# Optimization experiments

Hardware: AMD Instinct MI355X
Metric: run time of the kernel (lower is better)

## Reference

```python
import jax, jax.numpy as jnp
import numpy as np

C = 256   # channel
NH = 8    # n_heads
NP = 8    # n_points (n_levels = 1)
HD = C // NH


def conv1x1(x, W, b):
    # x: [B,C,H,W], W: [Cout,Cin] -> 1x1 conv == channel-mixing GEMM
    return jnp.einsum('bchw,oc->bohw', x, W) + b[None, :, None, None]


def linear(x, W, b):
    # x: [B,Q,Cin], W: [Cout,Cin] (torch nn.Linear layout)
    return jnp.einsum('bqc,oc->bqo', x, W) + b


def msda(value, loc, attn_w, H, Wd):
    # Multi-scale deformable attention core (single level).
    # value:  [B,Q,NH,HD]  (Q = H*Wd)
    # loc:    [B,Q,NH,NP,2] normalized sampling locations in [0,1] (x,y)
    # attn_w: [B,Q,NH,NP]  softmax weights
    B, Q = value.shape[0], value.shape[1]
    v = jnp.transpose(value, (0, 2, 1, 3))  # [B,NH,HW,HD]
    # grid_sample(align_corners=False): pixel coord = loc*size - 0.5
    ix = loc[..., 0] * Wd - 0.5
    iy = loc[..., 1] * H - 0.5
    x0 = jnp.floor(ix)
    y0 = jnp.floor(iy)

    def gather(xi, yi, wgt):
        valid = ((xi >= 0) & (xi < Wd) & (yi >= 0) & (yi < H)).astype(wgt.dtype)
        xc = jnp.clip(xi, 0, Wd - 1).astype(jnp.int32)
        yc = jnp.clip(yi, 0, H - 1).astype(jnp.int32)
        idx = yc * Wd + xc                                  # [B,Q,NH,NP]
        idx = jnp.transpose(idx, (0, 2, 1, 3)).reshape(B, NH, Q * NP)
        s = jnp.take_along_axis(v, idx[..., None], axis=2)  # [B,NH,Q*NP,HD]
        s = s.reshape(B, NH, Q, NP, HD)
        w = jnp.transpose(wgt * valid, (0, 2, 1, 3))[..., None]
        return s * w

    acc = (gather(x0, y0, (x0 + 1 - ix) * (y0 + 1 - iy))
           + gather(x0 + 1, y0, (ix - x0) * (y0 + 1 - iy))
           + gather(x0, y0 + 1, (x0 + 1 - ix) * (iy - y0))
           + gather(x0 + 1, y0 + 1, (ix - x0) * (iy - y0)))
    aw = jnp.transpose(attn_w, (0, 2, 1, 3))[..., None]      # [B,NH,Q,NP,1]
    out = (acc * aw).sum(axis=3)                             # [B,NH,Q,HD]
    return jnp.transpose(out, (0, 2, 1, 3)).reshape(B, Q, C)


def setup_inputs() -> dict:
    key = jax.random.key(0)
    ks = jax.random.split(key, 24)
    B, H, W = 2, 128, 128

    def w(k, shape, s=0.02):
        return jax.random.normal(k, shape, jnp.float32) * s

    d = {
        'xt': jax.random.normal(ks[0], (B, C, H, W), jnp.float32),
        'xt_1': jax.random.normal(ks[1], (B, C, H, W), jnp.float32),
        'W_in1': w(ks[2], (C, C)), 'b_in1': jnp.zeros((C,), jnp.float32),
        'W_in2': w(ks[3], (C, C)), 'b_in2': jnp.zeros((C,), jnp.float32),
        'Wv': w(ks[4], (C, C)), 'bv': jnp.zeros((C,), jnp.float32),
        'Ws': w(ks[5], (NH * NP * 2, C)), 'bs_off': w(ks[6], (NH * NP * 2,), 1.0),
        'Wa': w(ks[7], (NH * NP, C)), 'ba': jnp.zeros((NH * NP,), jnp.float32),
        'Wo': w(ks[8], (C, C)), 'bo': jnp.zeros((C,), jnp.float32),
        'Wt1': w(ks[9], (C, C)), 'bt1': jnp.zeros((C,), jnp.float32),
        'Wt2': w(ks[10], (C, C)), 'bt2': jnp.zeros((C,), jnp.float32),
        'Wout': w(ks[11], (C, C)), 'bout': jnp.zeros((C,), jnp.float32),
    }
    return d


def reference(xt, xt_1, W_in1, b_in1, W_in2, b_in2, Wv, bv, Ws, bs_off,
              Wa, ba, Wo, bo, Wt1, bt1, Wt2, bt2, Wout, bout):
    x1 = conv1x1(xt, W_in1, b_in1)
    x2 = conv1x1(xt_1, W_in2, b_in2)
    B, _, H, Wd = x1.shape
    Q = H * Wd
    q = jnp.transpose(x1, (0, 2, 3, 1)).reshape(B, Q, C)       # queries
    vflat = jnp.transpose(x2, (0, 2, 3, 1)).reshape(B, Q, C)   # values

    value = linear(vflat, Wv, bv).reshape(B, Q, NH, HD)
    offsets = linear(q, Ws, bs_off).reshape(B, Q, NH, NP, 2)
    attn = jax.nn.softmax(linear(q, Wa, ba).reshape(B, Q, NH, NP), axis=-1)

    # reference points at pixel centers, normalized (x,y)
    gy, gx = jnp.meshgrid(jnp.arange(H), jnp.arange(Wd), indexing='ij')
    ref = jnp.stack([(gx.reshape(-1) + 0.5) / Wd,
                     (gy.reshape(-1) + 0.5) / H], axis=-1).astype(jnp.float32)
    norm = jnp.array([Wd, H], jnp.float32)
    loc = ref[None, :, None, None, :] + offsets / norm          # [B,Q,NH,NP,2]

    out = msda(value, loc, attn, H, Wd)                         # [B,Q,C]
    xt_star = jnp.transpose(linear(out, Wo, bo), (0, 2, 1)).reshape(B, C, H, Wd)

    tg = conv1x1(jax.nn.relu(conv1x1(x1 * xt_star, Wt1, bt1)), Wt2, bt2)
    return jax.nn.relu(conv1x1(x1 + tg, Wout, bout))
```

## Files before the change

kernel.cpp:

```cpp
#include <hip/hip_runtime.h>
#include <math.h>


#define PIX 16384
#define BATCH 2
#define CH 256

typedef short bf16x8 __attribute__((ext_vector_type(8)));
typedef float f32x4 __attribute__((ext_vector_type(4)));

typedef const __attribute__((address_space(1))) void* as1cv;
typedef __attribute__((address_space(3))) void* as3v;
__device__ __forceinline__ void gl_lds16(const void* g, void* l) {
  __builtin_amdgcn_global_load_lds((as1cv)g, (as3v)l, 16, 0, 0);
}

__device__ __forceinline__ ushort f2bf(float f) {
  union { float f; unsigned u; } v; v.f = f;
  unsigned u = v.u;
  unsigned r = u + 0x7fffu + ((u >> 16) & 1u);
  return (ushort)(r >> 16);
}
__device__ __forceinline__ float bfl(unsigned u) {
  union { unsigned u; float f; } v; v.u = u << 16; return v.f;
}
__device__ __forceinline__ float bfh(unsigned u) {
  union { unsigned u; float f; } v; v.u = u & 0xffff0000u; return v.f;
}
__device__ __forceinline__ unsigned fuse_u32(unsigned a, unsigned b, bool mul) {
  float rl = mul ? bfl(a) * bfl(b) : bfl(a) + bfl(b);
  float rh = mul ? bfh(a) * bfh(b) : bfh(a) + bfh(b);
  return (unsigned)f2bf(rl) | ((unsigned)f2bf(rh) << 16);
}

__global__ __launch_bounds__(256) void wprep_k(
    const float* __restrict__ W_in1, const float* __restrict__ Wo,
    const float* __restrict__ Wt1, const float* __restrict__ Wt2,
    const float* __restrict__ Wout, const float* __restrict__ Ws,
    const float* __restrict__ Wa, const float* __restrict__ bs_off,
    const float* __restrict__ ba, ushort* __restrict__ wb,
    float* __restrict__ bsa)
{
  const int blk = blockIdx.x, k = threadIdx.x;
  if (blk >= 1472) {
    if (k < 128) bsa[k] = bs_off[k];
    else if (k < 192) bsa[k] = ba[k - 128];
    return;
  }
  const float* src;
  if (blk < 256) src = W_in1 + (size_t)blk * 256;
  else if (blk < 512) src = Wo + (size_t)(blk - 256) * 256;
  else if (blk < 768) src = Wt1 + (size_t)(blk - 512) * 256;
  else if (blk < 1024) src = Wt2 + (size_t)(blk - 768) * 256;
  else if (blk < 1280) src = Wout + (size_t)(blk - 1024) * 256;
  else if (blk < 1408) src = Ws + (size_t)(blk - 1280) * 256;
  else src = Wa + (size_t)(blk - 1408) * 256;
  wb[(size_t)blk * 256 + k] = f2bf(src[k]);
}

__global__ __launch_bounds__(256) void wvcomp_k(
    const float* __restrict__ Wv, const float* __restrict__ W_in2,
    const float* __restrict__ b_in2, const float* __restrict__ bv,
    ushort* __restrict__ Wvp, float* __restrict__ bvp)
{
  const int o = blockIdx.x, k = threadIdx.x;
  float acc = 0.f;
  #pragma unroll 8
  for (int c = 0; c < 256; ++c)
    acc += Wv[(size_t)o * 256 + c] * W_in2[(size_t)c * 256 + k];
  Wvp[(size_t)o * 256 + k] = f2bf(acc);
  __shared__ float red[256];
  red[k] = Wv[(size_t)o * 256 + k] * b_in2[k];
  __syncthreads();
  for (int s = 128; s > 0; s >>= 1) {
    if (k < s) red[k] += red[k + s];
    __syncthreads();
  }
  if (k == 0) bvp[o] = red[0] + bv[o];
}

__global__ __launch_bounds__(256) void tconv2_k(
    const float* __restrict__ inA, const float* __restrict__ inB,
    ushort* __restrict__ outA, ushort* __restrict__ outB)
{
  __shared__ float t[32][33];
  const int tid = threadIdx.x;
  const int z = blockIdx.z;
  const int b = z & 1;
  const float* in = (z < 2) ? inA : inB;
  ushort* out = (z < 2) ? outA : outB;
  const int p0 = blockIdx.x * 32, c0 = blockIdx.y * 32;
  const int tx = tid & 31, ty = tid >> 5;
  const float* inb = in + (size_t)b * CH * PIX;
  #pragma unroll
  for (int i = 0; i < 4; ++i)
    t[ty + i * 8][tx] = inb[(size_t)(c0 + ty + i * 8) * PIX + p0 + tx];
  __syncthreads();
  const int cx = (tid & 15) * 2, py = tid >> 4;
  ushort* outb = out + (size_t)b * PIX * CH;
  #pragma unroll
  for (int i = 0; i < 2; ++i) {
    int pl = py + i * 16;
    unsigned lo = f2bf(t[cx][pl]);
    unsigned hi = f2bf(t[cx + 1][pl]);
    *(unsigned*)(outb + (size_t)(p0 + pl) * CH + c0 + cx) = lo | (hi << 16);
  }
}

template<int FUSE, bool RELU, int OMODE>
__global__ __launch_bounds__(256, 3) void gemm2_k(
    const ushort* __restrict__ in, const ushort* __restrict__ in2,
    const ushort* __restrict__ Wb, const float* __restrict__ bias,
    void* __restrict__ out, int ldo, size_t obstride)
{
  __shared__ __align__(16) char smem[49152];
  const int tid = threadIdx.x;
  const int b = blockIdx.z;
  const int p0 = blockIdx.x * 128;
  const int o0 = blockIdx.y * 64;

  const ushort* inb = in + (size_t)b * PIX * CH;

  const int srow = tid >> 3, sseg = tid & 7;
  const int ssw = (srow & 7);
  const int gseg = (FUSE == 0) ? (sseg ^ ssw) : sseg;
  const ushort* xsrc = inb + (size_t)(p0 + srow) * CH + gseg * 8;
  const ushort* x2src = (FUSE != 0)
      ? in2 + (size_t)b * PIX * CH + (size_t)(p0 + srow) * CH + sseg * 8
      : (const ushort*)nullptr;
  const ushort* wsrc = Wb + (size_t)(o0 + srow) * CH + gseg * 8;

  const int l = tid & 63, wv = tid >> 6;
  const int lr = l & 15, g4 = l >> 4;

  f32x4 acc[2][4];
  #pragma unroll
  for (int i = 0; i < 2; ++i)
    #pragma unroll
    for (int j = 0; j < 4; ++j) acc[i][j] = (f32x4){0.f, 0.f, 0.f, 0.f};

  uint4 xr[4], x2r[4], wr[2];

#define STAGE_GLL(buf, kb)                                                     \
  {                                                                            \
    _Pragma("unroll")                                                          \
    for (int r = 0; r < 4; ++r)                                                \
      gl_lds16(xsrc + (kb) + (size_t)r * 32 * CH,                              \
               smem + (buf) * 16384 + r * 4096 + tid * 16);                    \
    _Pragma("unroll")                                                          \
    for (int r = 0; r < 2; ++r)                                                \
      gl_lds16(wsrc + (kb) + (size_t)r * 32 * CH,                              \
               smem + 32768 + (buf) * 8192 + r * 4096 + tid * 16);             \
  }

#define LOADT(kb)                                                              \
  {                                                                            \
    _Pragma("unroll")                                                          \
    for (int r = 0; r < 4; ++r)                                                \
      xr[r] = *(const uint4*)(xsrc + (kb) + (size_t)r * 32 * CH);              \
    _Pragma("unroll")                                                          \
    for (int r = 0; r < 4; ++r)                                                \
      x2r[r] = *(const uint4*)(x2src + (kb) + (size_t)r * 32 * CH);            \
    _Pragma("unroll")                                                          \
    for (int r = 0; r < 2; ++r)                                                \
      wr[r] = *(const uint4*)(wsrc + (kb) + (size_t)r * 32 * CH);              \
  }

#define WRITET(buf)                                                            \
  {                                                                            \
    _Pragma("unroll")                                                          \
    for (int r = 0; r < 4; ++r) {                                              \
      uint4 v = xr[r];                                                         \
      unsigned* pa = (unsigned*)&v;                                            \
      const unsigned* pb = (const unsigned*)&x2r[r];                           \
      _Pragma("unroll")                                                        \
      for (int w = 0; w < 4; ++w) pa[w] = fuse_u32(pa[w], pb[w], FUSE == 1);   \
      *(uint4*)(smem + (buf) * 16384 + (srow + r * 32) * 128 +                 \
                ((sseg ^ ssw) * 16)) = v;                                      \
    }                                                                          \
    _Pragma("unroll")                                                          \
    for (int r = 0; r < 2; ++r)                                                \
      *(uint4*)(smem + 32768 + (buf) * 8192 + (srow + r * 32) * 128 +          \
                ((sseg ^ ssw) * 16)) = wr[r];                                  \
  }

  if (FUSE == 0) { STAGE_GLL(0, 0) }
  else           { LOADT(0) WRITET(0) }
  __syncthreads();

  for (int t = 0; t < 4; ++t) {
    if (t < 3) {
      if (FUSE == 0) { STAGE_GLL((t + 1) & 1, (t + 1) * 64) }
      else           { LOADT((t + 1) * 64) }
    }
    const char* XB = smem + (t & 1) * 16384;
    const char* WB = smem + 32768 + (t & 1) * 8192;
    bf16x8 af[2][2], bfr[4][2];
    #pragma unroll
    for (int fm = 0; fm < 2; ++fm) {
      const int p = wv * 32 + fm * 16 + lr;
      #pragma unroll
      for (int kh = 0; kh < 2; ++kh)
        af[fm][kh] = *(const bf16x8*)(XB + p * 128 + (((kh * 4 + g4) ^ (p & 7)) * 16));
    }
    #pragma unroll
    for (int fn = 0; fn < 4; ++fn) {
      const int o = fn * 16 + lr;
      #pragma unroll
      for (int kh = 0; kh < 2; ++kh)
        bfr[fn][kh] = *(const bf16x8*)(WB + o * 128 + (((kh * 4 + g4) ^ (o & 7)) * 16));
    }
    #pragma unroll
    for (int fm = 0; fm < 2; ++fm)
      #pragma unroll
      for (int fn = 0; fn < 4; ++fn) {
        acc[fm][fn] = __builtin_amdgcn_mfma_f32_16x16x32_bf16(af[fm][0], bfr[fn][0], acc[fm][fn], 0, 0, 0);
        acc[fm][fn] = __builtin_amdgcn_mfma_f32_16x16x32_bf16(af[fm][1], bfr[fn][1], acc[fm][fn], 0, 0, 0);
      }
    if (t < 3 && FUSE != 0) { WRITET((t + 1) & 1) }
    __syncthreads();
  }
#undef STAGE_GLL
#undef LOADT
#undef WRITET

  float bvv[4];
  #pragma unroll
  for (int fn = 0; fn < 4; ++fn) bvv[fn] = bias[o0 + fn * 16 + lr];

  if (OMODE == 1) {
    float* El2 = (float*)smem;
    #pragma unroll
    for (int fm = 0; fm < 2; ++fm)
      #pragma unroll
      for (int fn = 0; fn < 4; ++fn) {
        float4 v;
        v.x = acc[fm][fn][0] + bvv[fn]; v.y = acc[fm][fn][1] + bvv[fn];
        v.z = acc[fm][fn][2] + bvv[fn]; v.w = acc[fm][fn][3] + bvv[fn];
        if (RELU) {
          v.x = fmaxf(v.x, 0.f); v.y = fmaxf(v.y, 0.f);
          v.z = fmaxf(v.z, 0.f); v.w = fmaxf(v.w, 0.f);
        }
        *(float4*)&El2[(size_t)(fn * 16 + lr) * 132 + wv * 32 + fm * 16 + g4 * 4] = v;
      }
    __syncthreads();
    float* outb = (float*)out + (size_t)b * obstride;
    const int og = tid >> 5, seg = tid & 31;
    #pragma unroll
    for (int r = 0; r < 8; ++r) {
      const int orow = og + r * 8;
      float4 v = *(float4*)(smem + orow * 528 + seg * 16);
      *(float4*)(outb + (size_t)(o0 + orow) * ldo + p0 + seg * 4) = v;
    }
  } else if (OMODE == 0) {
    ushort* El = (ushort*)smem;
    #pragma unroll
    for (int fm = 0; fm < 2; ++fm)
      #pragma unroll
      for (int fn = 0; fn < 4; ++fn)
        #pragma unroll
        for (int r = 0; r < 4; ++r) {
          const int p = wv * 32 + fm * 16 + g4 * 4 + r;
          float v = acc[fm][fn][r] + bvv[fn];
          if (RELU) v = fmaxf(v, 0.f);
          El[p * 72 + fn * 16 + lr] = f2bf(v);
        }
    __syncthreads();
    ushort* outb = (ushort*)out + (size_t)b * obstride;
    const int rg = tid >> 3, seg = tid & 7;
    #pragma unroll
    for (int r = 0; r < 4; ++r) {
      const int row = rg + r * 32;
      uint4 v = *(uint4*)(smem + row * 144 + seg * 16);
      *(uint4*)(outb + (size_t)(p0 + row) * ldo + o0 + seg * 8) = v;
    }
  } else {
    float* El = (float*)smem;
    #pragma unroll
    for (int fm = 0; fm < 2; ++fm)
      #pragma unroll
      for (int fn = 0; fn < 4; ++fn)
        #pragma unroll
        for (int r = 0; r < 4; ++r) {
          const int p = wv * 32 + fm * 16 + g4 * 4 + r;
          float v = acc[fm][fn][r] + bvv[fn];
          if (RELU) v = fmaxf(v, 0.f);
          El[p * 68 + fn * 16 + lr] = v;
        }
    __syncthreads();
    float* outb = (float*)out + (size_t)b * obstride;
    const int rg = tid >> 4, seg = tid & 15;
    #pragma unroll
    for (int r = 0; r < 8; ++r) {
      const int row = rg + r * 16;
      float4 v = *(float4*)(smem + row * 272 + seg * 16);
      *(float4*)(outb + (size_t)(p0 + row) * ldo + o0 + seg * 4) = v;
    }
  }
}

__global__ __launch_bounds__(256) void msda_k(
    const ushort* __restrict__ value, const float* __restrict__ sa,
    ushort* __restrict__ out)
{
  const int t = blockIdx.x * 256 + threadIdx.x;
  const int dh = t & 1;
  const int h = (t >> 1) & 7;
  const int pg = t >> 4;
  const int b = pg >> 14;
  const int p = pg & (PIX - 1);
  const int px = p & 127, py = p >> 7;

  const ushort* vb = value + (size_t)b * PIX * CH;
  const float* sp = sa + (size_t)pg * 192;

  float4 la = *(const float4*)(sp + 128 + h * 8);
  float4 lb = *(const float4*)(sp + 128 + h * 8 + 4);
  float lg[8] = {la.x, la.y, la.z, la.w, lb.x, lb.y, lb.z, lb.w};
  float m = lg[0];
  #pragma unroll
  for (int i = 1; i < 8; ++i) m = fmaxf(m, lg[i]);
  float s = 0.f;
  #pragma unroll
  for (int i = 0; i < 8; ++i) { lg[i] = __expf(lg[i] - m); s += lg[i]; }
  const float inv = 1.f / s;

  float of[16];
  #pragma unroll
  for (int j = 0; j < 4; ++j)
    *(float4*)&of[j * 4] = *(const float4*)(sp + h * 16 + j * 4);

  float acc[16];
  #pragma unroll
  for (int i = 0; i < 16; ++i) acc[i] = 0.f;

  #pragma unroll
  for (int pt = 0; pt < 8; ++pt) {
    const float ox = of[2 * pt], oy = of[2 * pt + 1];
    const float aw = lg[pt] * inv;
    const float ix = px + ox, iy = py + oy;
    const float xf = floorf(ix), yf = floorf(iy);
    const float fx = ix - xf, fy = iy - yf;
    const int x0 = (int)xf, y0 = (int)yf;
    #pragma unroll
    for (int cr = 0; cr < 4; ++cr) {
      const int dx = cr & 1, dy = cr >> 1;
      const int xx = x0 + dx, yy = y0 + dy;
      const float wx = dx ? fx : (1.f - fx);
      const float wy = dy ? fy : (1.f - fy);
      const bool valid = ((unsigned)xx < 128u) & ((unsigned)yy < 128u);
      float w = valid ? (wx * wy * aw) : 0.f;
      const int xc = min(max(xx, 0), 127), yc = min(max(yy, 0), 127);
      const ushort* vr = vb + ((size_t)(yc * 128 + xc) * CH + h * 32 + dh * 16);
      uint4 q0 = *(const uint4*)vr;
      uint4 q1 = *(const uint4*)(vr + 8);
      const unsigned* qw0 = (const unsigned*)&q0;
      const unsigned* qw1 = (const unsigned*)&q1;
      #pragma unroll
      for (int ww = 0; ww < 4; ++ww) {
        acc[2 * ww + 0] = fmaf(w, bfl(qw0[ww]), acc[2 * ww + 0]);
        acc[2 * ww + 1] = fmaf(w, bfh(qw0[ww]), acc[2 * ww + 1]);
        acc[8 + 2 * ww + 0] = fmaf(w, bfl(qw1[ww]), acc[8 + 2 * ww + 0]);
        acc[8 + 2 * ww + 1] = fmaf(w, bfh(qw1[ww]), acc[8 + 2 * ww + 1]);
      }
    }
  }
  unsigned r[8];
  #pragma unroll
  for (int k = 0; k < 8; ++k)
    r[k] = (unsigned)f2bf(acc[2 * k]) | ((unsigned)f2bf(acc[2 * k + 1]) << 16);
  ushort* dst = out + (size_t)pg * CH + h * 32 + dh * 16;
  *(uint4*)dst = *(uint4*)&r[0];
  *(uint4*)(dst + 8) = *(uint4*)&r[4];
}

extern "C" void kernel_launch(void* const* d_in, const int* in_sizes, int n_in,
                              void* d_out, int out_size, void* d_ws, size_t ws_size,
                              hipStream_t stream)
{
  const float* xt     = (const float*)d_in[0];
  const float* xt_1   = (const float*)d_in[1];
  const float* W_in1  = (const float*)d_in[2];
  const float* b_in1  = (const float*)d_in[3];
  const float* W_in2  = (const float*)d_in[4];
  const float* b_in2  = (const float*)d_in[5];
  const float* Wv     = (const float*)d_in[6];
  const float* bv     = (const float*)d_in[7];
  const float* Ws     = (const float*)d_in[8];
  const float* bs_off = (const float*)d_in[9];
  const float* Wa     = (const float*)d_in[10];
  const float* ba     = (const float*)d_in[11];
  const float* Wo     = (const float*)d_in[12];
  const float* bo     = (const float*)d_in[13];
  const float* Wt1    = (const float*)d_in[14];
  const float* bt1    = (const float*)d_in[15];
  const float* Wt2    = (const float*)d_in[16];
  const float* bt2    = (const float*)d_in[17];
  const float* Wout   = (const float*)d_in[18];
  const float* bout   = (const float*)d_in[19];

  char* ws = (char*)d_ws;
  const size_t SLOT = (size_t)BATCH * PIX * CH * 2;
  const size_t SAB  = (size_t)BATCH * PIX * 192 * 4;
  ushort* s0 = (ushort*)(ws + 0 * SLOT);
  ushort* s1 = (ushort*)(ws + 1 * SLOT);
  ushort* s2 = (ushort*)(ws + 2 * SLOT);
  ushort* s3 = (ushort*)(ws + 3 * SLOT);
  ushort* s4 = (ushort*)(ws + 4 * SLOT);
  float*  sa = (float*)(ws + 5 * SLOT);
  char* wbase = ws + 5 * SLOT + SAB;
  ushort* wb  = (ushort*)wbase;
  ushort* wvp = (ushort*)(wbase + (size_t)1472 * 256 * 2);
  float* bsa  = (float*)(wbase + (size_t)1472 * 256 * 2 + (size_t)256 * 256 * 2);
  float* bvp  = bsa + 192;

  ushort* wb_in1 = wb;
  ushort* wb_o   = wb + 65536;
  ushort* wb_t1  = wb + 131072;
  ushort* wb_t2  = wb + 196608;
  ushort* wb_out = wb + 262144;
  ushort* wb_sa  = wb + 327680;

  dim3 blk(256);
  dim3 gT(PIX / 32, CH / 32, 2 * BATCH);
  dim3 gF(PIX / 128, 4, BATCH);
  dim3 gS(PIX / 128, 3, BATCH);
  const size_t OBS = (size_t)PIX * CH;

  wprep_k<<<1473, blk, 0, stream>>>(W_in1, Wo, Wt1, Wt2, Wout, Ws, Wa, bs_off, ba, wb, bsa);
  wvcomp_k<<<256, blk, 0, stream>>>(Wv, W_in2, b_in2, bv, wvp, bvp);
  tconv2_k<<<gT, blk, 0, stream>>>(xt, xt_1, s0, s1);

  gemm2_k<0, false, 0><<<gF, blk, 0, stream>>>(s0, nullptr, wb_in1, b_in1, s2, CH, OBS);
  gemm2_k<0, false, 0><<<gF, blk, 0, stream>>>(s1, nullptr, wvp, bvp, s3, CH, OBS);
  gemm2_k<0, false, 2><<<gS, blk, 0, stream>>>(s2, nullptr, wb_sa, bsa, sa, 192, (size_t)PIX * 192);
  msda_k<<<dim3((BATCH * PIX * 16) / 256), blk, 0, stream>>>(s3, sa, s4);
  gemm2_k<0, false, 0><<<gF, blk, 0, stream>>>(s4, nullptr, wb_o, bo, s0, CH, OBS);
  gemm2_k<1, true , 0><<<gF, blk, 0, stream>>>(s0, s2, wb_t1, bt1, s1, CH, OBS);
  gemm2_k<0, false, 0><<<gF, blk, 0, stream>>>(s1, nullptr, wb_t2, bt2, s3, CH, OBS);
  gemm2_k<2, true , 1><<<gF, blk, 0, stream>>>(s3, s2, wb_out, bout, d_out, PIX, (size_t)CH * PIX);
}
```

Baseline: 164.9 us.

## Halve GEMM K-tile to cut LDS and store sampling params as bf16

The GEMM kernel moves from 64-wide to 32-wide K stages over eight iterations. This shrinks the shared-memory footprint with a matching swizzle, so four blocks per CU can be resident instead of three. Separately, the offset/attention-logit projection now writes bf16 instead of fp32, and msda_k decodes bf16 for those values. This halves that intermediate's traffic but lowers the precision of the sampling offsets and logits, and the shorter K stages add more barriers per block.

New measurement: 164.5 us. Within noise of the previous version (-0.2%).

```diff
diff --git a/kernel.cpp b/kernel.cpp
--- a/kernel.cpp
+++ b/kernel.cpp
@@ -108,12 +108,13 @@
 }
 
 template<int FUSE, bool RELU, int OMODE>
-__global__ __launch_bounds__(256, 3) void gemm2_k(
+__global__ __launch_bounds__(256, 4) void gemm2_k(
     const ushort* __restrict__ in, const ushort* __restrict__ in2,
     const ushort* __restrict__ Wb, const float* __restrict__ bias,
     void* __restrict__ out, int ldo, size_t obstride)
 {
-  __shared__ __align__(16) char smem[49152];
+  constexpr int SMEMSZ = (OMODE == 0) ? 24576 : 34816;
+  __shared__ __align__(16) char smem[SMEMSZ];
   const int tid = threadIdx.x;
   const int b = blockIdx.z;
   const int p0 = blockIdx.x * 128;
@@ -121,14 +122,19 @@
 
   const ushort* inb = in + (size_t)b * PIX * CH;
 
-  const int srow = tid >> 3, sseg = tid & 7;
-  const int ssw = (srow & 7);
-  const int gseg = (FUSE == 0) ? (sseg ^ ssw) : sseg;
-  const ushort* xsrc = inb + (size_t)(p0 + srow) * CH + gseg * 8;
-  const ushort* x2src = (FUSE != 0)
-      ? in2 + (size_t)b * PIX * CH + (size_t)(p0 + srow) * CH + sseg * 8
-      : (const ushort*)nullptr;
-  const ushort* wsrc = Wb + (size_t)(o0 + srow) * CH + gseg * 8;
+  const int srow = tid >> 2;
+  const int sseg = tid & 3;
+  const int swz0 = (srow >> 1) & 3;
+  const int swz1 = ((srow + 64) >> 1) & 3;
+  const int gseg0 = (FUSE == 0) ? (sseg ^ swz0) : sseg;
+  const int gseg1 = (FUSE == 0) ? (sseg ^ swz1) : sseg;
+  const ushort* xsrc0 = inb + (size_t)(p0 + srow) * CH + gseg0 * 8;
+  const ushort* xsrc1 = inb + (size_t)(p0 + srow + 64) * CH + gseg1 * 8;
+  const ushort* x2src0 = (FUSE != 0)
+      ? in2 + (size_t)b * PIX * CH + (size_t)(p0 + srow) * CH + sseg * 8 : (const ushort*)nullptr;
+  const ushort* x2src1 = (FUSE != 0)
+      ? in2 + (size_t)b * PIX * CH + (size_t)(p0 + srow + 64) * CH + sseg * 8 : (const ushort*)nullptr;
+  const ushort* wsrc = Wb + (size_t)(o0 + srow) * CH + gseg0 * 8;
 
   const int l = tid & 63, wv = tid >> 6;
   const int lr = l & 15, g4 = l >> 4;
@@ -139,85 +145,69 @@
     #pragma unroll
     for (int j = 0; j < 4; ++j) acc[i][j] = (f32x4){0.f, 0.f, 0.f, 0.f};
 
-  uint4 xr[4], x2r[4], wr[2];
+  uint4 xr[2], x2r[2], wr;
 
 #define STAGE_GLL(buf, kb)                                                     \
   {                                                                            \
-    _Pragma("unroll")                                                          \
-    for (int r = 0; r < 4; ++r)                                                \
-      gl_lds16(xsrc + (kb) + (size_t)r * 32 * CH,                              \
-               smem + (buf) * 16384 + r * 4096 + tid * 16);                    \
-    _Pragma("unroll")                                                          \
-    for (int r = 0; r < 2; ++r)                                                \
-      gl_lds16(wsrc + (kb) + (size_t)r * 32 * CH,                              \
-               smem + 32768 + (buf) * 8192 + r * 4096 + tid * 16);             \
+    gl_lds16(xsrc0 + (kb), smem + (buf) * 8192 + tid * 16);                    \
+    gl_lds16(xsrc1 + (kb), smem + (buf) * 8192 + 4096 + tid * 16);             \
+    gl_lds16(wsrc + (kb), smem + 16384 + (buf) * 4096 + tid * 16);             \
   }
 
 #define LOADT(kb)                                                              \
   {                                                                            \
-    _Pragma("unroll")                                                          \
-    for (int r = 0; r < 4; ++r)                                                \
-      xr[r] = *(const uint4*)(xsrc + (kb) + (size_t)r * 32 * CH);              \
-    _Pragma("unroll")                                                          \
-    for (int r = 0; r < 4; ++r)                                                \
-      x2r[r] = *(const uint4*)(x2src + (kb) + (size_t)r * 32 * CH);            \
-    _Pragma("unroll")                                                          \
-    for (int r = 0; r < 2; ++r)                                                \
-      wr[r] = *(const uint4*)(wsrc + (kb) + (size_t)r * 32 * CH);              \
+    xr[0] = *(const uint4*)(x2src0 ? xsrc0 + (kb) : xsrc0 + (kb));             \
+    xr[1] = *(const uint4*)(xsrc1 + (kb));                                     \
+    x2r[0] = *(const uint4*)(x2src0 + (kb));                                   \
+    x2r[1] = *(const uint4*)(x2src1 + (kb));                                   \
+    wr = *(const uint4*)(wsrc + (kb));                                         \
   }
 
 #define WRITET(buf)                                                            \
   {                                                                            \
     _Pragma("unroll")                                                          \
-    for (int r = 0; r < 4; ++r) {                                              \
+    for (int r = 0; r < 2; ++r) {                                              \
       uint4 v = xr[r];                                                         \
       unsigned* pa = (unsigned*)&v;                                            \
       const unsigned* pb = (const unsigned*)&x2r[r];                           \
       _Pragma("unroll")                                                        \
       for (int w = 0; w < 4; ++w) pa[w] = fuse_u32(pa[w], pb[w], FUSE == 1);   \
-      *(uint4*)(smem + (buf) * 16384 + (srow + r * 32) * 128 +                 \
-                ((sseg ^ ssw) * 16)) = v;                                      \
+      const int sw = r ? swz1 : swz0;                                          \
+      *(uint4*)(smem + (buf) * 8192 + r * 4096 + srow * 64 +                   \
+                ((sseg ^ sw) * 16)) = v;                                       \
     }                                                                          \
-    _Pragma("unroll")                                                          \
-    for (int r = 0; r < 2; ++r)                                                \
-      *(uint4*)(smem + 32768 + (buf) * 8192 + (srow + r * 32) * 128 +          \
-                ((sseg ^ ssw) * 16)) = wr[r];                                  \
+    *(uint4*)(smem + 16384 + (buf) * 4096 + srow * 64 +                        \
+              ((sseg ^ swz0) * 16)) = wr;                                      \
   }
 
   if (FUSE == 0) { STAGE_GLL(0, 0) }
   else           { LOADT(0) WRITET(0) }
   __syncthreads();
 
-  for (int t = 0; t < 4; ++t) {
-    if (t < 3) {
-      if (FUSE == 0) { STAGE_GLL((t + 1) & 1, (t + 1) * 64) }
-      else           { LOADT((t + 1) * 64) }
-    }
-    const char* XB = smem + (t & 1) * 16384;
-    const char* WB = smem + 32768 + (t & 1) * 8192;
-    bf16x8 af[2][2], bfr[4][2];
+  for (int t = 0; t < 8; ++t) {
+    if (t < 7) {
+      if (FUSE == 0) { STAGE_GLL((t + 1) & 1, (t + 1) * 32) }
+      else           { LOADT((t + 1) * 32) }
+    }
+    const char* XB = smem + (t & 1) * 8192;
+    const char* WB = smem + 16384 + (t & 1) * 4096;
+    bf16x8 af[2], bfr[4];
     #pragma unroll
     for (int fm = 0; fm < 2; ++fm) {
       const int p = wv * 32 + fm * 16 + lr;
-      #pragma unroll
-      for (int kh = 0; kh < 2; ++kh)
-        af[fm][kh] = *(const bf16x8*)(XB + p * 128 + (((kh * 4 + g4) ^ (p & 7)) * 16));
+      af[fm] = *(const bf16x8*)(XB + p * 64 + ((g4 ^ ((p >> 1) & 3)) * 16));
     }
     #pragma unroll
     for (int fn = 0; fn < 4; ++fn) {
       const int o = fn * 16 + lr;
-      #pragma unroll
-      for (int kh = 0; kh < 2; ++kh)
-        bfr[fn][kh] = *(const bf16x8*)(WB + o * 128 + (((kh * 4 + g4) ^ (o & 7)) * 16));
+      bfr[fn] = *(const bf16x8*)(WB + o * 64 + ((g4 ^ ((o >> 1) & 3)) * 16));
     }
     #pragma unroll
     for (int fm = 0; fm < 2; ++fm)
       #pragma unroll
-      for (int fn = 0; fn < 4; ++fn) {
-        acc[fm][fn] = __builtin_amdgcn_mfma_f32_16x16x32_bf16(af[fm][0], bfr[fn][0], acc[fm][fn], 0, 0, 0);
-        acc[fm][fn] = __builtin_amdgcn_mfma_f32_16x16x32_bf16(af[fm][1], bfr[fn][1], acc[fm][fn], 0, 0, 0);
-      }
-    if (t < 3 && FUSE != 0) { WRITET((t + 1) & 1) }
+      for (int fn = 0; fn < 4; ++fn)
+        acc[fm][fn] = __builtin_amdgcn_mfma_f32_16x16x32_bf16(af[fm], bfr[fn], acc[fm][fn], 0, 0, 0);
+    if (t < 7 && FUSE != 0) { WRITET((t + 1) & 1) }
     __syncthreads();
   }
 #undef STAGE_GLL
@@ -252,7 +242,7 @@
       float4 v = *(float4*)(smem + orow * 528 + seg * 16);
       *(float4*)(outb + (size_t)(o0 + orow) * ldo + p0 + seg * 4) = v;
     }
-  } else if (OMODE == 0) {
+  } else {
     ushort* El = (ushort*)smem;
     #pragma unroll
     for (int fm = 0; fm < 2; ++fm)
@@ -274,33 +264,11 @@
       uint4 v = *(uint4*)(smem + row * 144 + seg * 16);
       *(uint4*)(outb + (size_t)(p0 + row) * ldo + o0 + seg * 8) = v;
     }
-  } else {
-    float* El = (float*)smem;
-    #pragma unroll
-    for (int fm = 0; fm < 2; ++fm)
-      #pragma unroll
-      for (int fn = 0; fn < 4; ++fn)
-        #pragma unroll
-        for (int r = 0; r < 4; ++r) {
-          const int p = wv * 32 + fm * 16 + g4 * 4 + r;
-          float v = acc[fm][fn][r] + bvv[fn];
-          if (RELU) v = fmaxf(v, 0.f);
-          El[p * 68 + fn * 16 + lr] = v;
-        }
-    __syncthreads();
-    float* outb = (float*)out + (size_t)b * obstride;
-    const int rg = tid >> 4, seg = tid & 15;
-    #pragma unroll
-    for (int r = 0; r < 8; ++r) {
-      const int row = rg + r * 16;
-      float4 v = *(float4*)(smem + row * 272 + seg * 16);
-      *(float4*)(outb + (size_t)(p0 + row) * ldo + o0 + seg * 4) = v;
-    }
   }
 }
 
 __global__ __launch_bounds__(256) void msda_k(
-    const ushort* __restrict__ value, const float* __restrict__ sa,
+    const ushort* __restrict__ value, const ushort* __restrict__ sa,
     ushort* __restrict__ out)
 {
   const int t = blockIdx.x * 256 + threadIdx.x;
@@ -312,11 +280,13 @@
   const int px = p & 127, py = p >> 7;
 
   const ushort* vb = value + (size_t)b * PIX * CH;
-  const float* sp = sa + (size_t)pg * 192;
-
-  float4 la = *(const float4*)(sp + 128 + h * 8);
-  float4 lb = *(const float4*)(sp + 128 + h * 8 + 4);
-  float lg[8] = {la.x, la.y, la.z, la.w, lb.x, lb.y, lb.z, lb.w};
+  const ushort* sp = sa + (size_t)pg * 192;
+
+  uint4 lgv = *(const uint4*)(sp + 128 + h * 8);
+  const unsigned* lgw = (const unsigned*)&lgv;
+  float lg[8];
+  #pragma unroll
+  for (int i = 0; i < 4; ++i) { lg[2 * i] = bfl(lgw[i]); lg[2 * i + 1] = bfh(lgw[i]); }
   float m = lg[0];
   #pragma unroll
   for (int i = 1; i < 8; ++i) m = fmaxf(m, lg[i]);
@@ -325,10 +295,17 @@
   for (int i = 0; i < 8; ++i) { lg[i] = __expf(lg[i] - m); s += lg[i]; }
   const float inv = 1.f / s;
 
+  uint4 ov0 = *(const uint4*)(sp + h * 16);
+  uint4 ov1 = *(const uint4*)(sp + h * 16 + 8);
   float of[16];
-  #pragma unroll
-  for (int j = 0; j < 4; ++j)
-    *(float4*)&of[j * 4] = *(const float4*)(sp + h * 16 + j * 4);
+  {
+    const unsigned* ow = (const unsigned*)&ov0;
+    #pragma unroll
+    for (int i = 0; i < 4; ++i) { of[2 * i] = bfl(ow[i]); of[2 * i + 1] = bfh(ow[i]); }
+    const unsigned* ow1 = (const unsigned*)&ov1;
+    #pragma unroll
+    for (int i = 0; i < 4; ++i) { of[8 + 2 * i] = bfl(ow1[i]); of[8 + 2 * i + 1] = bfh(ow1[i]); }
+  }
 
   float acc[16];
   #pragma unroll
@@ -401,13 +378,13 @@
 
   char* ws = (char*)d_ws;
   const size_t SLOT = (size_t)BATCH * PIX * CH * 2;
-  const size_t SAB  = (size_t)BATCH * PIX * 192 * 4;
+  const size_t SAB  = (size_t)BATCH * PIX * 192 * 2;
   ushort* s0 = (ushort*)(ws + 0 * SLOT);
   ushort* s1 = (ushort*)(ws + 1 * SLOT);
   ushort* s2 = (ushort*)(ws + 2 * SLOT);
   ushort* s3 = (ushort*)(ws + 3 * SLOT);
   ushort* s4 = (ushort*)(ws + 4 * SLOT);
-  float*  sa = (float*)(ws + 5 * SLOT);
+  ushort* sa = (ushort*)(ws + 5 * SLOT);
   char* wbase = ws + 5 * SLOT + SAB;
   ushort* wb  = (ushort*)wbase;
   ushort* wvp = (ushort*)(wbase + (size_t)1472 * 256 * 2);
@@ -433,7 +410,7 @@
 
   gemm2_k<0, false, 0><<<gF, blk, 0, stream>>>(s0, nullptr, wb_in1, b_in1, s2, CH, OBS);
   gemm2_k<0, false, 0><<<gF, blk, 0, stream>>>(s1, nullptr, wvp, bvp, s3, CH, OBS);
-  gemm2_k<0, false, 2><<<gS, blk, 0, stream>>>(s2, nullptr, wb_sa, bsa, sa, 192, (size_t)PIX * 192);
+  gemm2_k<0, false, 0><<<gS, blk, 0, stream>>>(s2, nullptr, wb_sa, bsa, sa, 192, (size_t)PIX * 192);
   msda_k<<<dim3((BATCH * PIX * 16) / 256), blk, 0, stream>>>(s3, sa, s4);
   gemm2_k<0, false, 0><<<gF, blk, 0, stream>>>(s4, nullptr, wb_o, bo, s0, CH, OBS);
   gemm2_k<1, true , 0><<<gF, blk, 0, stream>>>(s0, s2, wb_t1, bt1, s1, CH, OBS);
```
